# Optimization experiments

Hardware: AMD Instinct MI355X
Metric: run time of the kernel (lower is better)

## Reference

```python
import jax, jax.numpy as jnp
import numpy as np

HEADS = 8
DIM_HEAD = 64
QUERY_DIM = 512
CONTEXT_DIM = 768
INNER_DIM = HEADS * DIM_HEAD  # 512
SCALE = DIM_HEAD ** -0.5


def setup_inputs() -> dict:
    key = jax.random.key(0)
    ks = jax.random.split(key, 7)
    B, N, M = 4, 2048, 1024
    x = jax.random.normal(ks[0], (B, N, QUERY_DIM), dtype=jnp.float32)
    context = jax.random.normal(ks[1], (B, M, CONTEXT_DIM), dtype=jnp.float32)
    # torch Linear weights stored as (out_features, in_features); y = x @ W.T
    Wq = jax.random.normal(ks[2], (INNER_DIM, QUERY_DIM), dtype=jnp.float32) * (QUERY_DIM ** -0.5)
    Wk = jax.random.normal(ks[3], (INNER_DIM, CONTEXT_DIM), dtype=jnp.float32) * (CONTEXT_DIM ** -0.5)
    Wv = jax.random.normal(ks[4], (INNER_DIM, CONTEXT_DIM), dtype=jnp.float32) * (CONTEXT_DIM ** -0.5)
    Wo = jax.random.normal(ks[5], (QUERY_DIM, INNER_DIM), dtype=jnp.float32) * (INNER_DIM ** -0.5)
    bo = jax.random.normal(ks[6], (QUERY_DIM,), dtype=jnp.float32) * 0.01
    return {"x": x, "context": context, "Wq": Wq, "Wk": Wk, "Wv": Wv, "Wo": Wo, "bo": bo}


def reference(x, context, Wq, Wk, Wv, Wo, bo):
    B, N, _ = x.shape
    M = context.shape[1]
    h, d = HEADS, DIM_HEAD
    q = jnp.einsum('bnc,ic->bni', x, Wq)        # [B,N,inner]
    k = jnp.einsum('bmc,ic->bmi', context, Wk)  # [B,M,inner]
    v = jnp.einsum('bmc,ic->bmi', context, Wv)  # [B,M,inner]
    # split heads: b n (h d) -> b h n d
    q = q.reshape(B, N, h, d).transpose(0, 2, 1, 3)
    k = k.reshape(B, M, h, d).transpose(0, 2, 1, 3)
    v = v.reshape(B, M, h, d).transpose(0, 2, 1, 3)
    # fp32 upcast for QK^T (inputs already fp32; kept explicit for fidelity)
    sim = jnp.einsum('bhnd,bhmd->bhnm', q.astype(jnp.float32), k.astype(jnp.float32)) * SCALE
    attn = jax.nn.softmax(sim, axis=-1)
    out = jnp.einsum('bhnm,bhmd->bhnd', attn, v)  # [B,h,N,d]
    out = out.transpose(0, 2, 1, 3).reshape(B, N, h * d)  # b n (h d)
    return jnp.einsum('bni,oi->bno', out, Wo) + bo  # dropout p=0 in eval
```

## Files before the change

### kernel.cpp

```cpp
#include <hip/hip_runtime.h>

using u16 = unsigned short;
typedef __bf16 bf16x8 __attribute__((ext_vector_type(8)));
typedef __bf16 bf16x2 __attribute__((ext_vector_type(2)));
typedef float  f32x4  __attribute__((ext_vector_type(4)));
typedef float  f32x16 __attribute__((ext_vector_type(16)));

#define MFMA16x16x32 __builtin_amdgcn_mfma_f32_16x16x32_bf16
#define MFMA32x32x16 __builtin_amdgcn_mfma_f32_32x32x16_bf16

#if __has_builtin(__builtin_amdgcn_exp2f)
#define EXP2 __builtin_amdgcn_exp2f
#else
#define EXP2 exp2f
#endif

static __device__ __forceinline__ unsigned f2bf_u(float f){
  unsigned x = __builtin_bit_cast(unsigned, f);
  return (x + 0x7fffu + ((x >> 16) & 1u)) >> 16;
}

static __device__ __forceinline__ void gll16(const void* g, void* l){
  __builtin_amdgcn_global_load_lds((const __attribute__((address_space(1))) void*)g,
                                   (__attribute__((address_space(3))) void*)l, 16, 0, 0);
}

static __device__ __forceinline__ f32x16 splat16(float x){
  f32x16 v;
#pragma unroll
  for (int i = 0; i < 16; ++i) v[i] = x;
  return v;
}

__global__ void __launch_bounds__(256) cvt_all(
    const float* __restrict__ x,  u16* __restrict__ xb,
    const float* __restrict__ cx, u16* __restrict__ cxb,
    const float* __restrict__ wq, u16* __restrict__ wqb,
    const float* __restrict__ wk, u16* __restrict__ wkb,
    const float* __restrict__ wv, u16* __restrict__ wvb,
    const float* __restrict__ wo, u16* __restrict__ wob)
{
  const float* in; u16* out; int n4;
  switch (blockIdx.y){
    case 0: in=x;  out=xb;  n4=(4*2048*512)/4; break;
    case 1: in=cx; out=cxb; n4=(4*1024*768)/4; break;
    case 2: in=wq; out=wqb; n4=(512*512)/4;    break;
    case 3: in=wk; out=wkb; n4=(512*768)/4;    break;
    case 4: in=wv; out=wvb; n4=(512*768)/4;    break;
    default:in=wo; out=wob; n4=(512*512)/4;    break;
  }
  int i = blockIdx.x*256 + threadIdx.x;
  const int stride = gridDim.x*256;
  for (; i < n4; i += stride){
    float4 f = ((const float4*)in)[i];
    ushort4 u;
    u.x = (u16)f2bf_u(f.x); u.y = (u16)f2bf_u(f.y);
    u.z = (u16)f2bf_u(f.z); u.w = (u16)f2bf_u(f.w);
    ((ushort4*)out)[i] = u;
  }
}

template<int LDA, int LDB, int KK, int OM>
static __device__ __forceinline__ void gemm_tile64(
    const u16* __restrict__ Ap, const u16* __restrict__ Bp,
    void* __restrict__ Cv, int ldc, int bx, int by,
    const float* __restrict__ bias, float scale,
    u16* __restrict__ sAp, u16* __restrict__ sBp)
{
  const int tid = threadIdx.x;
  const int w = tid >> 6, lane = tid & 63;
  const int wr = w >> 1, wc = w & 1;
  const long tm = (long)bx * 128;
  const long tn = (long)by * 64;

  f32x4 acc[4][2] = {};

  const int srl = lane >> 3, scc = lane & 7;

  auto stage = [&](int kt, int bb){
#pragma unroll
    for (int i = 0; i < 4; ++i){
      const int row = w*32 + i*8 + srl;
      const int sw = scc ^ (row & 7);
      gll16(Ap + (tm + row)*LDA + kt*64 + sw*8, sAp + bb*(128*64) + (w*32 + i*8)*64);
    }
#pragma unroll
    for (int i = 0; i < 2; ++i){
      const int row = w*16 + i*8 + srl;
      const int sw = scc ^ (row & 7);
      gll16(Bp + (tn + row)*LDB + kt*64 + sw*8, sBp + bb*(64*64) + (w*16 + i*8)*64);
    }
  };

  const int fr = lane & 15, fg = lane >> 4;
  constexpr int NK = KK / 64;

  stage(0, 0);
  __syncthreads();
  for (int kt = 0; kt < NK; ++kt){
    if (kt + 1 < NK) stage(kt + 1, (kt + 1) & 1);
    const int bb = kt & 1;
    bf16x8 af[4][2], bfr[2][2];
#pragma unroll
    for (int fm = 0; fm < 4; ++fm){
      const int row = wr*64 + fm*16 + fr;
      const int swz = row & 7;
#pragma unroll
      for (int s = 0; s < 2; ++s)
        af[fm][s] = *(const bf16x8*)&sAp[bb*(128*64) + row*64 + ((s*4 + fg) ^ swz)*8];
    }
#pragma unroll
    for (int fn = 0; fn < 2; ++fn){
      const int row = wc*32 + fn*16 + fr;
      const int swz = row & 7;
#pragma unroll
      for (int s = 0; s < 2; ++s)
        bfr[fn][s] = *(const bf16x8*)&sBp[bb*(64*64) + row*64 + ((s*4 + fg) ^ swz)*8];
    }
#pragma unroll
    for (int s = 0; s < 2; ++s)
#pragma unroll
      for (int fm = 0; fm < 4; ++fm)
#pragma unroll
        for (int fn = 0; fn < 2; ++fn)
          acc[fm][fn] = MFMA16x16x32(af[fm][s], bfr[fn][s], acc[fm][fn], 0, 0, 0);
    __syncthreads();
  }

#pragma unroll
  for (int fm = 0; fm < 4; ++fm){
#pragma unroll
    for (int fn = 0; fn < 2; ++fn){
      const long row0 = tm + wr*64 + fm*16 + fg*4;
      const long col  = tn + wc*32 + fn*16 + fr;
      if (OM == 0){
        u16* C = (u16*)Cv;
#pragma unroll
        for (int rr = 0; rr < 4; ++rr)
          C[(row0 + rr)*ldc + col] = (u16)f2bf_u(acc[fm][fn][rr] * scale);
      } else {
        float* C = (float*)Cv;
        const float bv = bias[col];
#pragma unroll
        for (int rr = 0; rr < 4; ++rr)
          C[(row0 + rr)*ldc + col] = acc[fm][fn][rr] + bv;
      }
    }
  }
}

template<int LDA, int LDB, int KK, int OM>
static __device__ __forceinline__ void gemm_tile128(
    const u16* __restrict__ Ap, const u16* __restrict__ Bp,
    void* __restrict__ Cv, int ldc, int bx, int by,
    const float* __restrict__ bias, float scale,
    u16* __restrict__ sAp, u16* __restrict__ sBp)
{
  const int tid = threadIdx.x;
  const int w = tid >> 6, lane = tid & 63;
  const int wr = w >> 1, wc = w & 1;
  const long tm = (long)bx * 128;
  const long tn = (long)by * 128;

  f32x4 acc[4][4] = {};

  const int srl = lane >> 3, scc = lane & 7;

  auto stage = [&](int kt, int bb){
#pragma unroll
    for (int i = 0; i < 4; ++i){
      const int row = w*32 + i*8 + srl;
      const int sw = scc ^ (row & 7);
      gll16(Ap + (tm + row)*LDA + kt*64 + sw*8, sAp + bb*(128*64) + (w*32 + i*8)*64);
      gll16(Bp + (tn + row)*LDB + kt*64 + sw*8, sBp + bb*(128*64) + (w*32 + i*8)*64);
    }
  };

  const int fr = lane & 15, fg = lane >> 4;
  constexpr int NK = KK / 64;

  stage(0, 0);
  __syncthreads();
  for (int kt = 0; kt < NK; ++kt){
    if (kt + 1 < NK) stage(kt + 1, (kt + 1) & 1);
    const int bb = kt & 1;
    bf16x8 af[4][2], bfr[4][2];
#pragma unroll
    for (int fm = 0; fm < 4; ++fm){
      const int row = wr*64 + fm*16 + fr;
      const int swz = row & 7;
#pragma unroll
      for (int s = 0; s < 2; ++s)
        af[fm][s] = *(const bf16x8*)&sAp[bb*(128*64) + row*64 + ((s*4 + fg) ^ swz)*8];
    }
#pragma unroll
    for (int fn = 0; fn < 4; ++fn){
      const int row = wc*64 + fn*16 + fr;
      const int swz = row & 7;
#pragma unroll
      for (int s = 0; s < 2; ++s)
        bfr[fn][s] = *(const bf16x8*)&sBp[bb*(128*64) + row*64 + ((s*4 + fg) ^ swz)*8];
    }
#pragma unroll
    for (int s = 0; s < 2; ++s)
#pragma unroll
      for (int fm = 0; fm < 4; ++fm)
#pragma unroll
        for (int fn = 0; fn < 4; ++fn)
          acc[fm][fn] = MFMA16x16x32(af[fm][s], bfr[fn][s], acc[fm][fn], 0, 0, 0);
    __syncthreads();
  }

#pragma unroll
  for (int fm = 0; fm < 4; ++fm){
#pragma unroll
    for (int fn = 0; fn < 4; ++fn){
      const long row0 = tm + wr*64 + fm*16 + fg*4;
      const long col  = tn + wc*64 + fn*16 + fr;
      if (OM == 0){
        u16* C = (u16*)Cv;
#pragma unroll
        for (int rr = 0; rr < 4; ++rr)
          C[(row0 + rr)*ldc + col] = (u16)f2bf_u(acc[fm][fn][rr] * scale);
      } else {
        float* C = (float*)Cv;
        const float bv = bias[col];
#pragma unroll
        for (int rr = 0; rr < 4; ++rr)
          C[(row0 + rr)*ldc + col] = acc[fm][fn][rr] + bv;
      }
    }
  }
}

__global__ __launch_bounds__(256, 2) void proj_fused(
    const u16* __restrict__ xb,  const u16* __restrict__ cxb,
    const u16* __restrict__ wqb, const u16* __restrict__ wkb,
    const u16* __restrict__ wvb,
    u16* __restrict__ qb, u16* __restrict__ kb, u16* __restrict__ vtb,
    float qscale)
{
  __shared__ u16 sA[2*128*64];
  __shared__ u16 sB[2*128*64];
  const int bid = blockIdx.x;
  const int lid = (bid & 7)*64 + (bid >> 3);
  if (lid < 256){
    gemm_tile128<512,512,512,0>(xb, wqb, (void*)qb, 512, lid >> 2, lid & 3,
                                nullptr, qscale, sA, sB);
  } else if (lid < 384){
    const int t = lid - 256;
    gemm_tile128<768,768,768,0>(cxb, wkb, (void*)kb, 512, t >> 2, t & 3,
                                nullptr, 1.0f, sA, sB);
  } else {
    const int t = lid - 384, z = t >> 5, r = t & 31;
    gemm_tile128<768,768,768,0>(wvb, cxb + (long)z*1024*768,
                                (void*)(vtb + (long)z*512*1024), 1024,
                                r >> 3, r & 7, nullptr, 1.0f, sA, sB);
  }
}

__global__ __launch_bounds__(256, 3) void gemm_out(
    const u16* __restrict__ ab, const u16* __restrict__ wob,
    float* __restrict__ out, const float* __restrict__ bias)
{
  __shared__ u16 sA[2*128*64];
  __shared__ u16 sB[2*64*64];
  const int bid = blockIdx.x;
  const int lid = (bid & 7)*64 + (bid >> 3);
  gemm_tile64<512,512,512,1>(ab, wob, (void*)out, 512, lid >> 3, lid & 7,
                             bias, 1.0f, sA, sB);
}

__global__ __launch_bounds__(256, 2) void attn_fwd(
    const u16* __restrict__ Q,
    const u16* __restrict__ Kb,
    const u16* __restrict__ Vt,
    u16* __restrict__ O)
{
  const int bid = blockIdx.x;
  const int lid = (bid & 7)*64 + (bid >> 3);
  const int qx = lid & 15, hh = (lid >> 4) & 7, b = lid >> 7;
  const int w = threadIdx.x >> 6, lane = threadIdx.x & 63;
  const int q31 = lane & 31, hi = lane >> 5;
  const int q0 = qx*128 + w*32;

  __shared__ u16 sK[4][64*64];
  __shared__ u16 sV[4][64*64];
  __shared__ float sLs[4*32];

  bf16x8 qf[4];
  {
    const u16* qrow = Q + (long)(b*2048 + q0 + q31)*512 + hh*64;
#pragma unroll
    for (int ks = 0; ks < 4; ++ks)
      qf[ks] = *(const bf16x8*)(qrow + ks*16 + hi*8);
  }

  f32x16 o[2] = {splat16(0.f), splat16(0.f)};
  float lsum = 0.f;

  const int srl = lane >> 3, scc = lane & 7;

  auto stage = [&](int kbv, int bb){
#pragma unroll
    for (int i = 0; i < 2; ++i){
      const int row = w*16 + i*8 + srl;
      const int sw = scc ^ (row & 7);
      gll16(Kb + (long)(b*1024 + kbv*64 + row)*512 + hh*64 + sw*8,
            &sK[bb][(w*16 + i*8)*64]);
      gll16(Vt + (long)(b*512 + hh*64 + row)*1024 + kbv*64 + sw*8,
            &sV[bb][(w*16 + i*8)*64]);
    }
  };

  stage(0, 0);
  stage(1, 1);

  for (int kb = 0; kb < 16; ++kb){
    if (kb + 2 < 16) stage(kb + 2, (kb + 2) & 3);
    if (kb <= 13)      asm volatile("s_waitcnt vmcnt(8)" ::: "memory");
    else if (kb == 14) asm volatile("s_waitcnt vmcnt(4)" ::: "memory");
    else               asm volatile("s_waitcnt vmcnt(0)" ::: "memory");
    __builtin_amdgcn_s_barrier();
    asm volatile("" ::: "memory");
    const u16* sKp = sK[kb & 3];
    const u16* sVp = sV[kb & 3];

    f32x16 sacc[2];
#pragma unroll
    for (int mt = 0; mt < 2; ++mt){
      sacc[mt] = splat16(-16.f);
      const int row = mt*32 + q31;
      const int swz = row & 7;
      __builtin_amdgcn_s_setprio(1);
#pragma unroll
      for (int ks = 0; ks < 4; ++ks){
        bf16x8 kf = *(const bf16x8*)&sKp[row*64 + ((ks*2 + hi) ^ swz)*8];
        sacc[mt] = MFMA32x32x16(kf, qf[ks], sacc[mt], 0, 0, 0);
      }
      __builtin_amdgcn_s_setprio(0);
    }

    unsigned pk[2][8];
#pragma unroll
    for (int mt = 0; mt < 2; ++mt){
#pragma unroll
      for (int r = 0; r < 16; ++r){
        sacc[mt][r] = EXP2(sacc[mt][r]);
        lsum += sacc[mt][r];
      }
#pragma unroll
      for (int p2 = 0; p2 < 8; ++p2){
        union { bf16x2 h; unsigned u; } t;
        t.h[0] = (__bf16)sacc[mt][2*p2];
        t.h[1] = (__bf16)sacc[mt][2*p2 + 1];
        pk[mt][p2] = t.u;
      }
    }

#pragma unroll
    for (int mt = 0; mt < 2; ++mt){
#pragma unroll
      for (int sl = 0; sl < 2; ++sl){
        const unsigned ca = pk[mt][sl*4 + 0], cb = pk[mt][sl*4 + 1];
        const unsigned cc = pk[mt][sl*4 + 2], cd = pk[mt][sl*4 + 3];
        const unsigned ya = hi ? ca : cc;
        const unsigned za = (unsigned)__shfl_xor((int)ya, 32);
        const unsigned yb = hi ? cb : cd;
        const unsigned zb = (unsigned)__shfl_xor((int)yb, 32);
        union { unsigned u[4]; bf16x8 v; } pa;
        pa.u[0] = hi ? za : ca;
        pa.u[1] = hi ? zb : cb;
        pa.u[2] = hi ? cc : za;
        pa.u[3] = hi ? cd : zb;
        const int s = mt*2 + sl;
        __builtin_amdgcn_s_setprio(1);
#pragma unroll
        for (int fd = 0; fd < 2; ++fd){
          const int row = fd*32 + q31;
          bf16x8 bv = *(const bf16x8*)&sVp[row*64 + (((s*2 + hi) ^ (row & 7)))*8];
          o[fd] = MFMA32x32x16(pa.v, bv, o[fd], 0, 0, 0);
        }
        __builtin_amdgcn_s_setprio(0);
      }
    }
    asm volatile("" ::: "memory");
  }

  lsum += __shfl_xor(lsum, 32);
  sLs[w*32 + q31] = lsum;
  __syncthreads();

  f32x4 inv[4];
#pragma unroll
  for (int g = 0; g < 4; ++g){
    f32x4 ls = *(const f32x4*)&sLs[w*32 + 8*g + 4*hi];
#pragma unroll
    for (int e = 0; e < 4; ++e) inv[g][e] = 1.0f / ls[e];
  }

  u16* orow = O + (long)(b*2048 + q0)*512 + hh*64;
#pragma unroll
  for (int fd = 0; fd < 2; ++fd){
#pragma unroll
    for (int r = 0; r < 16; ++r){
      const int q = (r & 3) + 8*(r >> 2) + 4*hi;
      const float val = o[fd][r] * inv[r >> 2][r & 3];
      orow[(long)q*512 + fd*32 + q31] = (u16)f2bf_u(val);
    }
  }
}

extern "C" void kernel_launch(void* const* d_in, const int* in_sizes, int n_in,
                              void* d_out, int out_size, void* d_ws, size_t ws_size,
                              hipStream_t stream)
{
  (void)in_sizes; (void)n_in; (void)out_size; (void)ws_size;
  const float* x   = (const float*)d_in[0];
  const float* ctx = (const float*)d_in[1];
  const float* Wq  = (const float*)d_in[2];
  const float* Wk  = (const float*)d_in[3];
  const float* Wv  = (const float*)d_in[4];
  const float* Wo  = (const float*)d_in[5];
  const float* bo  = (const float*)d_in[6];
  float* out = (float*)d_out;

  char* ws = (char*)d_ws;
  u16* xb  = (u16*)(ws + 0);
  u16* cxb = (u16*)(ws + 8388608);
  u16* wqb = (u16*)(ws + 14680064);
  u16* wkb = (u16*)(ws + 15204352);
  u16* wvb = (u16*)(ws + 15990784);
  u16* wob = (u16*)(ws + 16777216);
  u16* qb  = (u16*)(ws + 17301504);
  u16* kb  = (u16*)(ws + 25690112);
  u16* vtb = (u16*)(ws + 29884416);
  u16* ab  = (u16*)(ws + 34078720);

  cvt_all<<<dim3(1024, 6, 1), 256, 0, stream>>>(x, xb, ctx, cxb, Wq, wqb,
                                                Wk, wkb, Wv, wvb, Wo, wob);

  proj_fused<<<dim3(512, 1, 1), 256, 0, stream>>>(
      xb, cxb, wqb, wkb, wvb, qb, kb, vtb, 0.18033688011112042f);

  attn_fwd<<<dim3(512, 1, 1), 256, 0, stream>>>(qb, kb, vtb, ab);

  gemm_out<<<dim3(512, 1, 1), 256, 0, stream>>>(ab, wob, out, bo);
}
```

Measured before the change: 67.96 us.

## Process 64 query rows per wave in attention to reuse K/V tiles

Each wave in the attention kernel now handles two 32-row query sub-tiles instead of one, so each block covers 256 queries and the grid shrinks from 512 to 256 blocks. Every K fragment read from LDS feeds two QK MFMAs, every V fragment feeds two PV MFMAs, and the K/V global loads are shared by twice as many queries. The cost is roughly double the accumulator and register use (launch bounds drop to 1 block per SM) and fewer blocks than CUs on MI355X, which risks underfilling the GPU.

```diff
diff --git a/kernel.cpp b/kernel.cpp
--- a/kernel.cpp
+++ b/kernel.cpp
@@ -271,33 +271,34 @@
                              bias, 1.0f, sA, sB);
 }
 
-__global__ __launch_bounds__(256, 2) void attn_fwd(
+__global__ __launch_bounds__(256, 1) void attn_fwd(
     const u16* __restrict__ Q,
     const u16* __restrict__ Kb,
     const u16* __restrict__ Vt,
     u16* __restrict__ O)
 {
   const int bid = blockIdx.x;
-  const int lid = (bid & 7)*64 + (bid >> 3);
-  const int qx = lid & 15, hh = (lid >> 4) & 7, b = lid >> 7;
+  const int lid = (bid & 7)*32 + (bid >> 3);
+  const int qx = lid & 7, hh = (lid >> 3) & 7, b = lid >> 6;
   const int w = threadIdx.x >> 6, lane = threadIdx.x & 63;
   const int q31 = lane & 31, hi = lane >> 5;
-  const int q0 = qx*128 + w*32;
+  const int q0 = qx*256 + w*64;
 
   __shared__ u16 sK[4][64*64];
   __shared__ u16 sV[4][64*64];
-  __shared__ float sLs[4*32];
-
-  bf16x8 qf[4];
-  {
-    const u16* qrow = Q + (long)(b*2048 + q0 + q31)*512 + hh*64;
+  __shared__ float sLs[8*32];
+
+  bf16x8 qf[2][4];
+#pragma unroll
+  for (int j = 0; j < 2; ++j){
+    const u16* qrow = Q + (long)(b*2048 + q0 + j*32 + q31)*512 + hh*64;
 #pragma unroll
     for (int ks = 0; ks < 4; ++ks)
-      qf[ks] = *(const bf16x8*)(qrow + ks*16 + hi*8);
-  }
-
-  f32x16 o[2] = {splat16(0.f), splat16(0.f)};
-  float lsum = 0.f;
+      qf[j][ks] = *(const bf16x8*)(qrow + ks*16 + hi*8);
+  }
+
+  f32x16 o[2][2] = {{splat16(0.f), splat16(0.f)}, {splat16(0.f), splat16(0.f)}};
+  float lsum0 = 0.f, lsum1 = 0.f;
 
   const int srl = lane >> 3, scc = lane & 7;
 
@@ -326,60 +327,67 @@
     const u16* sKp = sK[kb & 3];
     const u16* sVp = sV[kb & 3];
 
-    f32x16 sacc[2];
 #pragma unroll
     for (int mt = 0; mt < 2; ++mt){
-      sacc[mt] = splat16(-16.f);
+      f32x16 s0 = splat16(-16.f), s1 = splat16(-16.f);
       const int row = mt*32 + q31;
       const int swz = row & 7;
       __builtin_amdgcn_s_setprio(1);
 #pragma unroll
       for (int ks = 0; ks < 4; ++ks){
         bf16x8 kf = *(const bf16x8*)&sKp[row*64 + ((ks*2 + hi) ^ swz)*8];
-        sacc[mt] = MFMA32x32x16(kf, qf[ks], sacc[mt], 0, 0, 0);
+        s0 = MFMA32x32x16(kf, qf[0][ks], s0, 0, 0, 0);
+        s1 = MFMA32x32x16(kf, qf[1][ks], s1, 0, 0, 0);
       }
       __builtin_amdgcn_s_setprio(0);
-    }
-
-    unsigned pk[2][8];
-#pragma unroll
-    for (int mt = 0; mt < 2; ++mt){
-#pragma unroll
-      for (int r = 0; r < 16; ++r){
-        sacc[mt][r] = EXP2(sacc[mt][r]);
-        lsum += sacc[mt][r];
-      }
+
+      unsigned pk0[8], pk1[8];
+#pragma unroll
+      for (int r = 0; r < 16; ++r){ s0[r] = EXP2(s0[r]); lsum0 += s0[r]; }
+#pragma unroll
+      for (int r = 0; r < 16; ++r){ s1[r] = EXP2(s1[r]); lsum1 += s1[r]; }
 #pragma unroll
       for (int p2 = 0; p2 < 8; ++p2){
-        union { bf16x2 h; unsigned u; } t;
-        t.h[0] = (__bf16)sacc[mt][2*p2];
-        t.h[1] = (__bf16)sacc[mt][2*p2 + 1];
-        pk[mt][p2] = t.u;
-      }
-    }
-
-#pragma unroll
-    for (int mt = 0; mt < 2; ++mt){
+        union { bf16x2 h; unsigned u; } t0, t1;
+        t0.h[0] = (__bf16)s0[2*p2]; t0.h[1] = (__bf16)s0[2*p2 + 1]; pk0[p2] = t0.u;
+        t1.h[0] = (__bf16)s1[2*p2]; t1.h[1] = (__bf16)s1[2*p2 + 1]; pk1[p2] = t1.u;
+      }
+
 #pragma unroll
       for (int sl = 0; sl < 2; ++sl){
-        const unsigned ca = pk[mt][sl*4 + 0], cb = pk[mt][sl*4 + 1];
-        const unsigned cc = pk[mt][sl*4 + 2], cd = pk[mt][sl*4 + 3];
-        const unsigned ya = hi ? ca : cc;
-        const unsigned za = (unsigned)__shfl_xor((int)ya, 32);
-        const unsigned yb = hi ? cb : cd;
-        const unsigned zb = (unsigned)__shfl_xor((int)yb, 32);
-        union { unsigned u[4]; bf16x8 v; } pa;
-        pa.u[0] = hi ? za : ca;
-        pa.u[1] = hi ? zb : cb;
-        pa.u[2] = hi ? cc : za;
-        pa.u[3] = hi ? cd : zb;
+        union { unsigned u[4]; bf16x8 v; } pa0, pa1;
+        {
+          const unsigned ca = pk0[sl*4 + 0], cb = pk0[sl*4 + 1];
+          const unsigned cc = pk0[sl*4 + 2], cd = pk0[sl*4 + 3];
+          const unsigned ya = hi ? ca : cc;
+          const unsigned za = (unsigned)__shfl_xor((int)ya, 32);
+          const unsigned yb = hi ? cb : cd;
+          const unsigned zb = (unsigned)__shfl_xor((int)yb, 32);
+          pa0.u[0] = hi ? za : ca;
+          pa0.u[1] = hi ? zb : cb;
+          pa0.u[2] = hi ? cc : za;
+          pa0.u[3] = hi ? cd : zb;
+        }
+        {
+          const unsigned ca = pk1[sl*4 + 0], cb = pk1[sl*4 + 1];
+          const unsigned cc = pk1[sl*4 + 2], cd = pk1[sl*4 + 3];
+          const unsigned ya = hi ? ca : cc;
+          const unsigned za = (unsigned)__shfl_xor((int)ya, 32);
+          const unsigned yb = hi ? cb : cd;
+          const unsigned zb = (unsigned)__shfl_xor((int)yb, 32);
+          pa1.u[0] = hi ? za : ca;
+          pa1.u[1] = hi ? zb : cb;
+          pa1.u[2] = hi ? cc : za;
+          pa1.u[3] = hi ? cd : zb;
+        }
         const int s = mt*2 + sl;
         __builtin_amdgcn_s_setprio(1);
 #pragma unroll
         for (int fd = 0; fd < 2; ++fd){
-          const int row = fd*32 + q31;
-          bf16x8 bv = *(const bf16x8*)&sVp[row*64 + (((s*2 + hi) ^ (row & 7)))*8];
-          o[fd] = MFMA32x32x16(pa.v, bv, o[fd], 0, 0, 0);
+          const int vrow = fd*32 + q31;
+          bf16x8 bv = *(const bf16x8*)&sVp[vrow*64 + (((s*2 + hi) ^ (vrow & 7)))*8];
+          o[0][fd] = MFMA32x32x16(pa0.v, bv, o[0][fd], 0, 0, 0);
+          o[1][fd] = MFMA32x32x16(pa1.v, bv, o[1][fd], 0, 0, 0);
         }
         __builtin_amdgcn_s_setprio(0);
       }
@@ -387,26 +395,30 @@
     asm volatile("" ::: "memory");
   }
 
-  lsum += __shfl_xor(lsum, 32);
-  sLs[w*32 + q31] = lsum;
+  lsum0 += __shfl_xor(lsum0, 32);
+  lsum1 += __shfl_xor(lsum1, 32);
+  sLs[(w*2 + 0)*32 + q31] = lsum0;
+  sLs[(w*2 + 1)*32 + q31] = lsum1;
   __syncthreads();
 
-  f32x4 inv[4];
-#pragma unroll
-  for (int g = 0; g < 4; ++g){
-    f32x4 ls = *(const f32x4*)&sLs[w*32 + 8*g + 4*hi];
-#pragma unroll
-    for (int e = 0; e < 4; ++e) inv[g][e] = 1.0f / ls[e];
-  }
-
-  u16* orow = O + (long)(b*2048 + q0)*512 + hh*64;
-#pragma unroll
-  for (int fd = 0; fd < 2; ++fd){
-#pragma unroll
-    for (int r = 0; r < 16; ++r){
-      const int q = (r & 3) + 8*(r >> 2) + 4*hi;
-      const float val = o[fd][r] * inv[r >> 2][r & 3];
-      orow[(long)q*512 + fd*32 + q31] = (u16)f2bf_u(val);
+#pragma unroll
+  for (int j = 0; j < 2; ++j){
+    f32x4 inv[4];
+#pragma unroll
+    for (int g = 0; g < 4; ++g){
+      f32x4 ls = *(const f32x4*)&sLs[(w*2 + j)*32 + 8*g + 4*hi];
+#pragma unroll
+      for (int e = 0; e < 4; ++e) inv[g][e] = 1.0f / ls[e];
+    }
+    u16* orow = O + (long)(b*2048 + q0 + j*32)*512 + hh*64;
+#pragma unroll
+    for (int fd = 0; fd < 2; ++fd){
+#pragma unroll
+      for (int r = 0; r < 16; ++r){
+        const int q = (r & 3) + 8*(r >> 2) + 4*hi;
+        const float val = o[j][fd][r] * inv[r >> 2][r & 3];
+        orow[(long)q*512 + fd*32 + q31] = (u16)f2bf_u(val);
+      }
     }
   }
 }
@@ -443,7 +455,7 @@
   proj_fused<<<dim3(512, 1, 1), 256, 0, stream>>>(
       xb, cxb, wqb, wkb, wvb, qb, kb, vtb, 0.18033688011112042f);
 
-  attn_fwd<<<dim3(512, 1, 1), 256, 0, stream>>>(qb, kb, vtb, ab);
+  attn_fwd<<<dim3(256, 1, 1), 256, 0, stream>>>(qb, kb, vtb, ab);
 
   gemm_out<<<dim3(512, 1, 1), 256, 0, stream>>>(ab, wob, out, bo);
 }
```

Result: slower. 77.16 us (+13.5%).
